# Performance work log

Hardware: AMD Instinct MI355X
Metric: run time of the kernel (lower is better)

The kernel has to match this reference:

```python
import jax, jax.numpy as jnp
import numpy as np

N = 4096      # n_nodes
IN = 256      # in_features
H = 4         # n_heads
F = 64        # out_features (per head)
SLOPE = 0.2   # leaky relu negative slope


def setup_inputs() -> dict:
    key = jax.random.key(0)
    k0, k1, k2, k3 = jax.random.split(key, 4)
    h = jax.random.normal(k0, (N, IN), dtype=jnp.float32)
    adj = jax.random.randint(k1, (N, N), 0, 2, dtype=jnp.int32)
    # ensure every node has at least one neighbor (self-loop) so softmax is defined
    adj = jnp.maximum(adj, jnp.eye(N, dtype=jnp.int32))
    # linear: in_features -> out_features * n_heads (xavier-ish scale)
    W = jax.random.normal(k2, (H * F, IN), dtype=jnp.float32) * np.float32(1.0 / np.sqrt(IN))
    b = jnp.zeros((H * F,), dtype=jnp.float32)
    # attn: Linear(2*F -> 1), weight row vector of size 2F plus scalar bias
    attn_w = jax.random.normal(k3, (2 * F,), dtype=jnp.float32) * np.float32(1.0 / np.sqrt(2 * F))
    attn_b = jnp.zeros((1,), dtype=jnp.float32)
    return {"h": h, "adj_mat": adj, "W": W, "b": b, "attn_w": attn_w, "attn_b": attn_b}


def reference(h, adj_mat, W, b, attn_w, attn_b):
    n = h.shape[0]
    # node projection: [N, H, F]
    g = (h @ W.T + b).reshape(n, H, F)
    # attn(concat(h_i, h_j)) = <a_src, g_i> + <a_dst, g_j> + bias  (decomposed, same math)
    src = jnp.einsum('nhf,f->nh', g, attn_w[:F])   # [N, H] contribution of node i
    dst = jnp.einsum('nhf,f->nh', g, attn_w[F:])   # [N, H] contribution of node j
    e = src[:, None, :] + dst[None, :, :] + attn_b[0]   # [N, N, H]
    e = jnp.where(e >= 0, e, SLOPE * e)                 # leaky relu
    e = jnp.where(adj_mat[:, :, None] != 0, e, -jnp.inf)  # mask non-edges
    a = jax.nn.softmax(e, axis=1)                       # softmax over neighbors j
    out = jnp.einsum('ijh,jhf->ihf', a, g)              # [N, H, F]
    return out.mean(axis=1)                             # average heads -> [N, F]
```

## Files before the change

kernel.cpp:

```cpp
#include <hip/hip_runtime.h>
#include <stdint.h>

constexpr int NODES = 4096;
constexpr int KIN   = 256;
constexpr int NHEAD = 4;
constexpr int NF    = 64;
constexpr int HFQ   = 256;
#define L2E 1.44269504088896340736f

typedef __attribute__((ext_vector_type(8))) short short8;
typedef __attribute__((ext_vector_type(4))) float floatx4;

static __device__ __forceinline__ unsigned short f2bf(float f) {
  return __builtin_bit_cast(unsigned short, (__bf16)f);
}

__global__ __launch_bounds__(256) void prep_kernel(
    const int* __restrict__ adj, unsigned* __restrict__ bm,
    const float* __restrict__ hin, const float* __restrict__ Win,
    const float* __restrict__ bias, const float* __restrict__ attn_w,
    const float* __restrict__ attn_b,
    unsigned short* __restrict__ gT3, float2* __restrict__ srcP,
    unsigned* __restrict__ eP) {
  __shared__ float2 sred[4][16];
  __shared__ unsigned pk[32][17];
  int tid = threadIdx.x;
  if (blockIdx.x < 1024) {
    int it = blockIdx.x >> 2, jq = blockIdx.x & 3;
    int i0 = it * 16;
    int wave = tid >> 6, lane = tid & 63;
    int lsh = (lane & 7) * 4;
#pragma unroll
    for (int rr = 0; rr < 4; ++rr) {
      int rloc = wave * 4 + rr;
      const int4* arow = reinterpret_cast<const int4*>(
          adj + (size_t)(i0 + rloc) * NODES + jq * 1024) + lane;
#pragma unroll
      for (int seg = 0; seg < 4; ++seg) {
        int4 a = arow[seg * 64];
        unsigned nib = (a.x != 0 ? 1u : 0u) | (a.y != 0 ? 2u : 0u)
                     | (a.z != 0 ? 4u : 0u) | (a.w != 0 ? 8u : 0u);
        unsigned wp = nib << lsh;
        wp |= (unsigned)__shfl_xor((int)wp, 1, 64);
        wp |= (unsigned)__shfl_xor((int)wp, 2, 64);
        wp |= (unsigned)__shfl_xor((int)wp, 4, 64);
        if ((lane & 7) == 0)
          pk[seg * 8 + (lane >> 3)][rloc] = wp;
      }
    }
    __syncthreads();
#pragma unroll
    for (int pass = 0; pass < 2; ++pass) {
      int idx = pass * 256 + tid;
      int jwl = idx >> 4, il = idx & 15;
      bm[(size_t)(jq * 32 + jwl) * NODES + i0 + il] = pk[jwl][il];
    }
    return;
  }
  int bid = blockIdx.x - 1024;
  int nt = tid >> 6, lane = tid & 63;
  int mt = bid >> 2, h = bid & 3;
  int m0 = mt * 16;
  int r = lane & 15, kg = lane >> 4;
  int col = h * NF + nt * 16 + r;
  floatx4 acc = {0.f, 0.f, 0.f, 0.f};
  const float* Af = hin + (m0 + r) * KIN + kg * 8;
  const float* Bf = Win + col * KIN + kg * 8;
#pragma unroll
  for (int kb = 0; kb < 8; ++kb) {
    float4 fa0 = *reinterpret_cast<const float4*>(Af + kb * 32);
    float4 fa1 = *reinterpret_cast<const float4*>(Af + kb * 32 + 4);
    float4 fb0 = *reinterpret_cast<const float4*>(Bf + kb * 32);
    float4 fb1 = *reinterpret_cast<const float4*>(Bf + kb * 32 + 4);
    short8 a, b;
    a[0] = (short)f2bf(fa0.x); a[1] = (short)f2bf(fa0.y);
    a[2] = (short)f2bf(fa0.z); a[3] = (short)f2bf(fa0.w);
    a[4] = (short)f2bf(fa1.x); a[5] = (short)f2bf(fa1.y);
    a[6] = (short)f2bf(fa1.z); a[7] = (short)f2bf(fa1.w);
    b[0] = (short)f2bf(fb0.x); b[1] = (short)f2bf(fb0.y);
    b[2] = (short)f2bf(fb0.z); b[3] = (short)f2bf(fb0.w);
    b[4] = (short)f2bf(fb1.x); b[5] = (short)f2bf(fb1.y);
    b[6] = (short)f2bf(fb1.z); b[7] = (short)f2bf(fb1.w);
    acc = __builtin_amdgcn_mfma_f32_16x16x32_bf16(a, b, acc, 0, 0, 0);
  }
  float bv = bias[col];
  float was = attn_w[nt * 16 + r], wad = attn_w[64 + nt * 16 + r];
  float ps[4], pd[4];
#pragma unroll
  for (int q = 0; q < 4; ++q) {
    int row = m0 + kg * 4 + q;
    float v = acc[q] + bv;
    int si = (row >> 5) * 8192 + h * 2048 + nt * 512 +
             (((row >> 3) & 3) * 16 + r) * 8 + (row & 7);
    gT3[si] = f2bf(v);
    ps[q] = v * was;
    pd[q] = v * wad;
  }
#pragma unroll
  for (int m = 8; m >= 1; m >>= 1)
#pragma unroll
    for (int q = 0; q < 4; ++q) {
      ps[q] += __shfl_xor(ps[q], m, 64);
      pd[q] += __shfl_xor(pd[q], m, 64);
    }
  if ((lane & 15) == 0)
#pragma unroll
    for (int q = 0; q < 4; ++q)
      sred[nt][kg * 4 + q] = float2{ps[q], pd[q]};
  __syncthreads();
  if (tid < 16) {
    int row = tid;
    float s = sred[0][row].x + sred[1][row].x + sred[2][row].x + sred[3][row].x + attn_b[0];
    float d = sred[0][row].y + sred[1][row].y + sred[2][row].y + sred[3][row].y;
    float2 sp;
    sp.x = exp2f(s * L2E);
    sp.y = exp2f(0.2f * s * L2E);
    srcP[(m0 + row) * NHEAD + h] = sp;
    float e1 = exp2f(d * L2E), e2 = exp2f(0.2f * d * L2E);
    eP[h * NODES + m0 + row] = ((unsigned)f2bf(e2) << 16) | (unsigned)f2bf(e1);
  }
}

__global__ __launch_bounds__(256, 8) void attn_kernel(
    const unsigned* __restrict__ bm, const unsigned short* __restrict__ gT3,
    const float2* __restrict__ srcP, const unsigned* __restrict__ eP,
    float* __restrict__ pnum, float* __restrict__ pden, int JP) {
  int tid = threadIdx.x;
  int hh = tid >> 6, lane = tid & 63;
  int il = lane & 15, kg = lane >> 4;
  int part = blockIdx.x, itile = blockIdx.y;
  int jstart = part * JP;
  int i = itile * 16 + il;

  float2 sp = srcP[i * NHEAD + hh];
  float es1 = sp.x, es2 = sp.y;

  floatx4 acc0 = {0.f, 0.f, 0.f, 0.f};
  floatx4 acc1 = acc0, acc2 = acc0, acc3 = acc0, accd = acc0;

  short8 ones;
#pragma unroll
  for (int r = 0; r < 8; ++r) ones[r] = (short)0x3F80;

  int jt0 = jstart >> 5;
  const unsigned* bmp = bm + (size_t)jt0 * NODES + i;
  const unsigned* epp = eP + hh * NODES + jstart + kg * 8;
  const unsigned short* Atp = gT3 + (size_t)jt0 * 8192 + hh * 2048 + lane * 8;

  unsigned mwd = *bmp;
  uint4 ea = *reinterpret_cast<const uint4*>(epp);
  uint4 eb = *reinterpret_cast<const uint4*>(epp + 4);

  int nsteps = JP / 32;

#define STEP_BODY {                                                         \
    unsigned mb = (mwd >> (kg * 8)) & 0xFFu;                                \
    unsigned ev[8] = {ea.x, ea.y, ea.z, ea.w, eb.x, eb.y, eb.z, eb.w};      \
    short8 bfr;                                                             \
    _Pragma("unroll")                                                       \
    for (int r = 0; r < 8; ++r) {                                           \
      float e1f = __builtin_bit_cast(float, ev[r] << 16);                   \
      float e2f = __builtin_bit_cast(float, ev[r] & 0xFFFF0000u);           \
      float w = fmaxf(es1 * e1f, es2 * e2f);                                \
      w = (mb & (1u << r)) ? w : 0.f;                                       \
      bfr[r] = (short)f2bf(w);                                              \
    }                                                                       \
    const short8 a0 = *reinterpret_cast<const short8*>(Atp);                \
    const short8 a1 = *reinterpret_cast<const short8*>(Atp + 512);          \
    const short8 a2 = *reinterpret_cast<const short8*>(Atp + 1024);         \
    const short8 a3 = *reinterpret_cast<const short8*>(Atp + 1536);         \
    acc0 = __builtin_amdgcn_mfma_f32_16x16x32_bf16(a0, bfr, acc0, 0, 0, 0); \
    acc1 = __builtin_amdgcn_mfma_f32_16x16x32_bf16(a1, bfr, acc1, 0, 0, 0); \
    acc2 = __builtin_amdgcn_mfma_f32_16x16x32_bf16(a2, bfr, acc2, 0, 0, 0); \
    acc3 = __builtin_amdgcn_mfma_f32_16x16x32_bf16(a3, bfr, acc3, 0, 0, 0); \
    accd = __builtin_amdgcn_mfma_f32_16x16x32_bf16(ones, bfr, accd, 0, 0, 0);\
  }

  for (int stp = 0; stp < nsteps - 1; ++stp) {
    unsigned mwd_n = bmp[NODES];
    uint4 ea_n = *reinterpret_cast<const uint4*>(epp + 32);
    uint4 eb_n = *reinterpret_cast<const uint4*>(epp + 36);
    STEP_BODY;
    mwd = mwd_n; ea = ea_n; eb = eb_n;
    bmp += NODES; epp += 32; Atp += 8192;
  }
  STEP_BODY;
#undef STEP_BODY

  if (kg == 0)
    pden[(size_t)part * (NODES * NHEAD) + i * NHEAD + hh] = accd[0];

  float* pbase = pnum + (size_t)part * (NODES * HFQ) + (size_t)i * HFQ + hh * NF;
#pragma unroll
  for (int q = 0; q < 4; ++q) {
    int c = kg * 4 + q;
    pbase[c] = acc0[q];
    pbase[16 + c] = acc1[q];
    pbase[32 + c] = acc2[q];
    pbase[48 + c] = acc3[q];
  }
}

__global__ __launch_bounds__(256) void combine_kernel(
    const float* __restrict__ pnum, const float* __restrict__ pden,
    float* __restrict__ out, int NP) {
  int idx = blockIdx.x * 256 + threadIdx.x;
  int i = idx >> 6, f = idx & 63;
  float o = 0.f;
#pragma unroll
  for (int hh = 0; hh < NHEAD; ++hh) {
    float num = 0.f, den = 0.f;
    for (int p = 0; p < NP; ++p) {
      num += pnum[p * (NODES * HFQ) + i * HFQ + hh * NF + f];
      den += pden[p * (NODES * NHEAD) + i * NHEAD + hh];
    }
    o += num / den;
  }
  out[idx] = 0.25f * o;
}

extern "C" void kernel_launch(void* const* d_in, const int* in_sizes, int n_in,
                              void* d_out, int out_size, void* d_ws, size_t ws_size,
                              hipStream_t stream) {
  const float* hin = (const float*)d_in[0];
  const int* adj   = (const int*)d_in[1];
  const float* W   = (const float*)d_in[2];
  const float* b   = (const float*)d_in[3];
  const float* aw  = (const float*)d_in[4];
  const float* ab  = (const float*)d_in[5];
  float* out = (float*)d_out;
  char* ws = (char*)d_ws;

  unsigned short* gT3 = (unsigned short*)(ws + 0x000000);
  float2* srcP        = (float2*)(ws + 0x200000);
  unsigned* eP        = (unsigned*)(ws + 0x220000);
  unsigned* bm        = (unsigned*)(ws + 0x240000);
  float* pden         = (float*)(ws + 0x440000);
  float* pnum         = (float*)(ws + 0x500000);
  const size_t base = 0x500000;

  int NP = 2;
  if (ws_size >= base + 8ull * NODES * HFQ * 4) NP = 8;
  else if (ws_size >= base + 4ull * NODES * HFQ * 4) NP = 4;
  int JP = NODES / NP;

  prep_kernel<<<2048, 256, 0, stream>>>(adj, bm, hin, W, b, aw, ab, gT3, srcP, eP);
  attn_kernel<<<dim3(NP, 256), 256, 0, stream>>>(bm, gT3, srcP, eP, pnum, pden, JP);
  combine_kernel<<<1024, 256, 0, stream>>>(pnum, pden, out, NP);
}
```

Baseline: 70.83 us.

## Share per-head feature tile across waves via double-buffered LDS

Each attention block is remapped so that one block handles a single head for 64 rows, instead of four heads for 16 rows. The four waves now share the same 32x64 bf16 feature tile, which is staged once per step into a double-buffered LDS array rather than loaded from global memory separately by each wave. This is meant to cut repeated global/L2 traffic for the MFMA A operand and to prefetch the next tile while the current one is used. In exchange it adds a __syncthreads barrier on every step and LDS usage that could limit occupancy.

Result: slower. 121.1 us (+71.0%).

```diff
diff --git a/kernel.cpp b/kernel.cpp
--- a/kernel.cpp
+++ b/kernel.cpp
@@ -125,12 +125,14 @@
     const unsigned* __restrict__ bm, const unsigned short* __restrict__ gT3,
     const float2* __restrict__ srcP, const unsigned* __restrict__ eP,
     float* __restrict__ pnum, float* __restrict__ pden, int JP) {
+  __shared__ unsigned short At_lds[2][2048];
   int tid = threadIdx.x;
-  int hh = tid >> 6, lane = tid & 63;
+  int wave = tid >> 6, lane = tid & 63;
   int il = lane & 15, kg = lane >> 4;
-  int part = blockIdx.x, itile = blockIdx.y;
+  int part = blockIdx.x;
+  int hh = blockIdx.y & 3, it64 = blockIdx.y >> 2;
   int jstart = part * JP;
-  int i = itile * 16 + il;
+  int i = it64 * 64 + wave * 16 + il;
 
   float2 sp = srcP[i * NHEAD + hh];
   float es1 = sp.x, es2 = sp.y;
@@ -145,47 +147,59 @@
   int jt0 = jstart >> 5;
   const unsigned* bmp = bm + (size_t)jt0 * NODES + i;
   const unsigned* epp = eP + hh * NODES + jstart + kg * 8;
-  const unsigned short* Atp = gT3 + (size_t)jt0 * 8192 + hh * 2048 + lane * 8;
-
+  const unsigned short* gsrc = gT3 + (size_t)jt0 * 8192 + hh * 2048 + tid * 8;
+
+  {
+    short8 st = *reinterpret_cast<const short8*>(gsrc);
+    *reinterpret_cast<short8*>(&At_lds[0][tid * 8]) = st;
+  }
   unsigned mwd = *bmp;
   uint4 ea = *reinterpret_cast<const uint4*>(epp);
   uint4 eb = *reinterpret_cast<const uint4*>(epp + 4);
+  __syncthreads();
 
   int nsteps = JP / 32;
-
-#define STEP_BODY {                                                         \
-    unsigned mb = (mwd >> (kg * 8)) & 0xFFu;                                \
-    unsigned ev[8] = {ea.x, ea.y, ea.z, ea.w, eb.x, eb.y, eb.z, eb.w};      \
-    short8 bfr;                                                             \
-    _Pragma("unroll")                                                       \
-    for (int r = 0; r < 8; ++r) {                                           \
-      float e1f = __builtin_bit_cast(float, ev[r] << 16);                   \
-      float e2f = __builtin_bit_cast(float, ev[r] & 0xFFFF0000u);           \
-      float w = fmaxf(es1 * e1f, es2 * e2f);                                \
-      w = (mb & (1u << r)) ? w : 0.f;                                       \
-      bfr[r] = (short)f2bf(w);                                              \
-    }                                                                       \
-    const short8 a0 = *reinterpret_cast<const short8*>(Atp);                \
-    const short8 a1 = *reinterpret_cast<const short8*>(Atp + 512);          \
-    const short8 a2 = *reinterpret_cast<const short8*>(Atp + 1024);         \
-    const short8 a3 = *reinterpret_cast<const short8*>(Atp + 1536);         \
-    acc0 = __builtin_amdgcn_mfma_f32_16x16x32_bf16(a0, bfr, acc0, 0, 0, 0); \
-    acc1 = __builtin_amdgcn_mfma_f32_16x16x32_bf16(a1, bfr, acc1, 0, 0, 0); \
-    acc2 = __builtin_amdgcn_mfma_f32_16x16x32_bf16(a2, bfr, acc2, 0, 0, 0); \
-    acc3 = __builtin_amdgcn_mfma_f32_16x16x32_bf16(a3, bfr, acc3, 0, 0, 0); \
-    accd = __builtin_amdgcn_mfma_f32_16x16x32_bf16(ones, bfr, accd, 0, 0, 0);\
-  }
-
-  for (int stp = 0; stp < nsteps - 1; ++stp) {
-    unsigned mwd_n = bmp[NODES];
-    uint4 ea_n = *reinterpret_cast<const uint4*>(epp + 32);
-    uint4 eb_n = *reinterpret_cast<const uint4*>(epp + 36);
-    STEP_BODY;
-    mwd = mwd_n; ea = ea_n; eb = eb_n;
-    bmp += NODES; epp += 32; Atp += 8192;
-  }
-  STEP_BODY;
-#undef STEP_BODY
+  for (int stp = 0; stp < nsteps; ++stp) {
+    int cur = stp & 1;
+    bool more = (stp + 1 < nsteps);
+    short8 stg;
+    unsigned mwd_n = 0;
+    uint4 ea_n, eb_n;
+    if (more) {
+      gsrc += 8192;
+      stg = *reinterpret_cast<const short8*>(gsrc);
+      mwd_n = bmp[NODES];
+      ea_n = *reinterpret_cast<const uint4*>(epp + 32);
+      eb_n = *reinterpret_cast<const uint4*>(epp + 36);
+    }
+    unsigned mb = (mwd >> (kg * 8)) & 0xFFu;
+    unsigned ev[8] = {ea.x, ea.y, ea.z, ea.w, eb.x, eb.y, eb.z, eb.w};
+    short8 bfr;
+#pragma unroll
+    for (int r = 0; r < 8; ++r) {
+      float e1f = __builtin_bit_cast(float, ev[r] << 16);
+      float e2f = __builtin_bit_cast(float, ev[r] & 0xFFFF0000u);
+      float w = fmaxf(es1 * e1f, es2 * e2f);
+      w = (mb & (1u << r)) ? w : 0.f;
+      bfr[r] = (short)f2bf(w);
+    }
+    const unsigned short* lp = &At_lds[cur][lane * 8];
+    const short8 a0 = *reinterpret_cast<const short8*>(lp);
+    const short8 a1 = *reinterpret_cast<const short8*>(lp + 512);
+    const short8 a2 = *reinterpret_cast<const short8*>(lp + 1024);
+    const short8 a3 = *reinterpret_cast<const short8*>(lp + 1536);
+    acc0 = __builtin_amdgcn_mfma_f32_16x16x32_bf16(a0, bfr, acc0, 0, 0, 0);
+    acc1 = __builtin_amdgcn_mfma_f32_16x16x32_bf16(a1, bfr, acc1, 0, 0, 0);
+    acc2 = __builtin_amdgcn_mfma_f32_16x16x32_bf16(a2, bfr, acc2, 0, 0, 0);
+    acc3 = __builtin_amdgcn_mfma_f32_16x16x32_bf16(a3, bfr, acc3, 0, 0, 0);
+    accd = __builtin_amdgcn_mfma_f32_16x16x32_bf16(ones, bfr, accd, 0, 0, 0);
+    if (more) {
+      *reinterpret_cast<short8*>(&At_lds[cur ^ 1][tid * 8]) = stg;
+      mwd = mwd_n; ea = ea_n; eb = eb_n;
+      bmp += NODES; epp += 32;
+      __syncthreads();
+    }
+  }
 
   if (kg == 0)
     pden[(size_t)part * (NODES * NHEAD) + i * NHEAD + hh] = accd[0];
```
